# Performance work log

Measured on AMD Instinct MI355X. Metric: run time of the kernel, lower is better.

Reference implementation:

```python
import jax, jax.numpy as jnp
import numpy as np

NUM_HEADS = 16
HEAD_SIZE = 64
EMB = NUM_HEADS * HEAD_SIZE
B, S = 2, 2048


def setup_inputs() -> dict:
    key = jax.random.key(0)
    ks = jax.random.split(key, 8)
    return {
        "values": jax.random.normal(ks[0], (B, S, EMB), dtype=jnp.float32),
        "keys": jax.random.normal(ks[1], (B, S, EMB), dtype=jnp.float32),
        "queries": jax.random.normal(ks[2], (B, S, EMB), dtype=jnp.float32),
        "mask": jnp.ones((B, 1, 1, S), dtype=jnp.int32),
        "Wq": jax.random.normal(ks[3], (HEAD_SIZE, HEAD_SIZE), dtype=jnp.float32) / np.sqrt(HEAD_SIZE),
        "Wk": jax.random.normal(ks[4], (HEAD_SIZE, HEAD_SIZE), dtype=jnp.float32) / np.sqrt(HEAD_SIZE),
        "Wv": jax.random.normal(ks[5], (HEAD_SIZE, HEAD_SIZE), dtype=jnp.float32) / np.sqrt(HEAD_SIZE),
        "Wout": jax.random.normal(ks[6], (EMB, EMB), dtype=jnp.float32) / np.sqrt(EMB),
        "bout": jax.random.normal(ks[7], (EMB,), dtype=jnp.float32) * 0.01,
    }


def reference(values, keys, queries, mask, Wq, Wk, Wv, Wout, bout):
    n, q_len, E = queries.shape
    H, D = NUM_HEADS, HEAD_SIZE
    # split heads: [n, len, H, D]
    v = values.reshape(n, -1, H, D)
    k = keys.reshape(n, -1, H, D)
    q = queries.reshape(n, q_len, H, D)
    # per-head shared linears (torch Linear: x @ W.T), no bias
    v = jnp.einsum("nkhd,cd->nkhc", v, Wv)
    k = jnp.einsum("nkhd,cd->nkhc", k, Wk)
    q = jnp.einsum("nqhd,cd->nqhc", q, Wq)
    # scores: [n, H, q, k]
    energy = jnp.einsum("nqhd,nkhd->nhqk", q, k)
    energy = jnp.where(mask == 0, jnp.float32(-1e28), energy)
    # NOTE: source scales by sqrt(embedding_size), not head_size
    attn = jax.nn.softmax(energy / jnp.sqrt(jnp.float32(E)), axis=3)
    out = jnp.einsum("nhqk,nkhd->nqhd", attn, v).reshape(n, q_len, E)
    return out @ Wout.T + bout
```

## Files before the change

kernel.cpp:

```cpp
#include <hip/hip_runtime.h>
#include <hip/hip_bf16.h>


#define NHB 16
#define HS  64
#define EMB 1024
#define BB  2
#define SS  2048
#define NT  (SS / 64)

typedef __bf16 bf16_t;
typedef bf16_t bf16x8 __attribute__((ext_vector_type(8)));
typedef bf16_t bf16x4 __attribute__((ext_vector_type(4)));
typedef float  f32x4  __attribute__((ext_vector_type(4)));

__device__ __forceinline__ f32x4 mfma16(bf16x8 a, bf16x8 b, f32x4 c) {
    return __builtin_amdgcn_mfma_f32_16x16x32_bf16(a, b, c, 0, 0, 0);
}

__device__ __forceinline__ float fast_exp2(float x) {
#if __has_builtin(__builtin_amdgcn_exp2f)
    return __builtin_amdgcn_exp2f(x);
#else
    float r;
    asm("v_exp_f32 %0, %1" : "=v"(r) : "v"(x));
    return r;
#endif
}

__global__ __launch_bounds__(512) void proj_kernel(
    const float* __restrict__ queries, const float* __restrict__ keys,
    const float* __restrict__ values,
    const float* __restrict__ Wq, const float* __restrict__ Wk,
    const float* __restrict__ Wv,
    bf16_t* __restrict__ Qb, bf16_t* __restrict__ Kb, bf16_t* __restrict__ Vt)
{
    __shared__ bf16_t Ws[3][64][72];
    __shared__ bf16_t Xs[128][72];

    const int tid  = threadIdx.x;
    const int wave = tid >> 6, lane = tid & 63;
    const int q4 = lane >> 4, l16 = lane & 15;
    const int s0 = blockIdx.x * 128;
    const int h  = blockIdx.y, n = blockIdx.z;

    #pragma unroll
    for (int i = 0; i < 6; ++i) {
        int g = i * 512 + tid;
        int mW = g >> 10;
        int idx4 = g & 1023;
        const float* wp = (mW == 0) ? Wq : (mW == 1) ? Wk : Wv;
        float4 v = ((const float4*)wp)[idx4];
        int r = idx4 >> 4, c = (idx4 & 15) * 4;
        Ws[mW][r][c+0] = (bf16_t)v.x; Ws[mW][r][c+1] = (bf16_t)v.y;
        Ws[mW][r][c+2] = (bf16_t)v.z; Ws[mW][r][c+3] = (bf16_t)v.w;
    }

    const size_t headBase = (size_t)(n * NHB + h) * SS * HS;

    float4 gx[4];
    auto loadX = [&](const float* xp) {
        #pragma unroll
        for (int i = 0; i < 4; ++i) {
            int idx4 = i * 512 + tid;
            int r = idx4 >> 4, c = (idx4 & 15) * 4;
            gx[i] = *(const float4*)&xp[((size_t)(n * SS + s0 + r)) * EMB + h * HS + c];
        }
    };
    loadX(queries);

    for (int p = 0; p < 3; ++p) {
        __syncthreads();
        #pragma unroll
        for (int i = 0; i < 4; ++i) {
            int idx4 = i * 512 + tid;
            int r = idx4 >> 4, c = (idx4 & 15) * 4;
            Xs[r][c+0] = (bf16_t)gx[i].x; Xs[r][c+1] = (bf16_t)gx[i].y;
            Xs[r][c+2] = (bf16_t)gx[i].z; Xs[r][c+3] = (bf16_t)gx[i].w;
        }
        if (p == 0) loadX(keys);
        else if (p == 1) loadX(values);
        __syncthreads();

        bf16x8 xf[2], wf[4][2];
        #pragma unroll
        for (int kk = 0; kk < 2; ++kk)
            xf[kk] = *(const bf16x8*)&Xs[wave * 16 + l16][kk * 32 + q4 * 8];
        #pragma unroll
        for (int ct = 0; ct < 4; ++ct)
            #pragma unroll
            for (int kk = 0; kk < 2; ++kk)
                wf[ct][kk] = *(const bf16x8*)&Ws[p][ct * 16 + l16][kk * 32 + q4 * 8];

        if (p < 2) {
            bf16_t* dst = (p == 0) ? Qb : Kb;
            const float sc = (p == 0) ? (0.03125f * 1.44269504f) : 1.0f;
            bf16x8 lo, hi;
            #pragma unroll
            for (int ct = 0; ct < 4; ++ct) {
                f32x4 acc = {};
                acc = mfma16(wf[ct][0], xf[0], acc);
                acc = mfma16(wf[ct][1], xf[1], acc);
                #pragma unroll
                for (int i = 0; i < 4; ++i) {
                    bf16_t v = (bf16_t)(acc[i] * sc);
                    if (ct < 2) lo[ct * 4 + i] = v;
                    else        hi[(ct - 2) * 4 + i] = v;
                }
            }
            bf16_t* rp = dst + headBase
                + (size_t)(s0 + wave * 16 + l16) * HS + q4 * 16;
            *(bf16x8*)rp = lo;
            *(bf16x8*)(rp + 8) = hi;
        } else {
            #pragma unroll
            for (int ct = 0; ct < 4; ++ct) {
                f32x4 acc = {};
                acc = mfma16(xf[0], wf[ct][0], acc);
                acc = mfma16(xf[1], wf[ct][1], acc);
                bf16x4 pk;
                #pragma unroll
                for (int i = 0; i < 4; ++i) pk[i] = (bf16_t)acc[i];
                *(bf16x4*)&Vt[headBase + (size_t)(ct * 16 + l16) * SS
                              + s0 + (wave >> 1) * 32 + q4 * 8 + (wave & 1) * 4] = pk;
            }
        }
    }
}

__global__ __launch_bounds__(512) void attn_kernel(
    const bf16_t* __restrict__ Qb, const bf16_t* __restrict__ Kb,
    const bf16_t* __restrict__ Vt, const int* __restrict__ mask,
    bf16_t* __restrict__ Og)
{
    __shared__ __align__(16) unsigned char smem[37376];
    auto Ks = (bf16_t(*)[64][72])(smem);
    auto Vs = (bf16_t(*)[64][72])(smem + 18432);
    auto Ms = (float(*)[64])(smem + 36864);
    float* fbuf = (float*)smem;
    float* lbuf = (float*)(smem + 32768);

    const int tid = threadIdx.x;
    const int w = tid >> 6, lane = tid & 63;
    const int q4 = lane >> 4, l16 = lane & 15;
    const int wq = w & 3, wk = w >> 2;
    const int qt = blockIdx.x, h = blockIdx.y, n = blockIdx.z;
    const size_t headBase = (size_t)(n * NHB + h) * SS * HS;
    const int* mrow = mask + n * SS;

    const int sr = tid >> 3, sc = (tid & 7) * 8;
    const bf16_t* kb_src = Kb + headBase + (size_t)sr * HS + sc;
    const bf16_t* vt_src = Vt + headBase + (size_t)sr * SS + sc;

    bf16x8 bq[2][2];
    #pragma unroll
    for (int st = 0; st < 2; ++st) {
        const bf16_t* qptr = Qb + headBase
            + (size_t)(qt * 128 + wq * 32 + st * 16 + l16) * HS;
        bq[st][0] = *(const bf16x8*)&qptr[q4 * 8];
        bq[st][1] = *(const bf16x8*)&qptr[32 + q4 * 8];
    }

    bf16x8 ones;
    #pragma unroll
    for (int i = 0; i < 8; ++i) ones[i] = (bf16_t)1.0f;

    f32x4 oaccT[2][4] = {};
    f32x4 lacc[2] = {};

    *(bf16x8*)&Ks[0][sr][sc] = *(const bf16x8*)kb_src;
    *(bf16x8*)&Vs[0][sr][sc] = *(const bf16x8*)vt_src;
    if (tid < 64) Ms[0][tid] = mrow[tid] ? 0.0f : -3e38f;
    __syncthreads();

    for (int kt = 0; kt < NT; ++kt) {
        const int cur = kt & 1;
        const bool has_next = (kt + 1) < NT;
        bf16x8 gk, gv; float gm = 0.f;
        if (has_next) {
            const int k0n = (kt + 1) * 64;
            gk = *(const bf16x8*)(kb_src + (size_t)k0n * HS);
            gv = *(const bf16x8*)(vt_src + k0n);
            if (tid < 64) gm = mrow[k0n + tid] ? 0.0f : -3e38f;
        }

        f32x4 sacc[2][2];
        #pragma unroll
        for (int c2 = 0; c2 < 2; ++c2) {
            const int ct = wk * 2 + c2;
            float4 bias = *(const float4*)&Ms[cur][ct * 16 + q4 * 4];
            f32x4 b4 = {bias.x, bias.y, bias.z, bias.w};
            sacc[0][c2] = b4; sacc[1][c2] = b4;
            bf16x8 ak0 = *(const bf16x8*)&Ks[cur][ct * 16 + l16][q4 * 8];
            bf16x8 ak1 = *(const bf16x8*)&Ks[cur][ct * 16 + l16][32 + q4 * 8];
            #pragma unroll
            for (int st = 0; st < 2; ++st) {
                sacc[st][c2] = mfma16(ak0, bq[st][0], sacc[st][c2]);
                sacc[st][c2] = mfma16(ak1, bq[st][1], sacc[st][c2]);
            }
        }

        bf16x4 pv[2][2];
        #pragma unroll
        for (int c2 = 0; c2 < 2; ++c2)
            #pragma unroll
            for (int st = 0; st < 2; ++st) {
                bf16x4 pk;
                #pragma unroll
                for (int j = 0; j < 4; ++j)
                    pk[j] = (bf16_t)fast_exp2(sacc[st][c2][j]);
                pv[st][c2] = pk;
            }

        bf16x8 pa[2];
        #pragma unroll
        for (int st = 0; st < 2; ++st)
            pa[st] = __builtin_shufflevector(pv[st][0], pv[st][1],
                                             0, 1, 2, 3, 4, 5, 6, 7);
        #pragma unroll
        for (int dt = 0; dt < 4; ++dt) {
            bf16x8 av = *(const bf16x8*)&Vs[cur][dt * 16 + l16][wk * 32 + q4 * 8];
            oaccT[0][dt] = mfma16(av, pa[0], oaccT[0][dt]);
            oaccT[1][dt] = mfma16(av, pa[1], oaccT[1][dt]);
        }
        lacc[0] = mfma16(ones, pa[0], lacc[0]);
        lacc[1] = mfma16(ones, pa[1], lacc[1]);

        if (has_next) {
            const int nxt = 1 - cur;
            *(bf16x8*)&Ks[nxt][sr][sc] = gk;
            *(bf16x8*)&Vs[nxt][sr][sc] = gv;
            if (tid < 64) Ms[nxt][tid] = gm;
        }
        __syncthreads();
    }

    float ls[2] = {lacc[0][0], lacc[1][0]};

    if (w >= 4) {
        const int lanecol = wq * 64 + lane;
        #pragma unroll
        for (int st = 0; st < 2; ++st) {
            #pragma unroll
            for (int dt = 0; dt < 4; ++dt)
                #pragma unroll
                for (int j = 0; j < 4; ++j)
                    fbuf[(st * 16 + dt * 4 + j) * 256 + lanecol] = oaccT[st][dt][j];
            lbuf[st * 256 + lanecol] = ls[st];
        }
    }
    __syncthreads();
    if (w < 4) {
        const int lanecol = wq * 64 + lane;
        #pragma unroll
        for (int st = 0; st < 2; ++st) {
            #pragma unroll
            for (int dt = 0; dt < 4; ++dt)
                #pragma unroll
                for (int j = 0; j < 4; ++j)
                    oaccT[st][dt][j] += fbuf[(st * 16 + dt * 4 + j) * 256 + lanecol];
            ls[st] += lbuf[st * 256 + lanecol];
        }
        #pragma unroll
        for (int st = 0; st < 2; ++st) {
            const float inv = 1.f / ls[st];
            const int qrow = qt * 128 + wq * 32 + st * 16 + l16;
            bf16_t* obase = Og + ((size_t)(n * SS + qrow)) * EMB + h * HS;
            #pragma unroll
            for (int dt = 0; dt < 4; ++dt) {
                bf16x4 ov;
                #pragma unroll
                for (int j = 0; j < 4; ++j) ov[j] = (bf16_t)(oaccT[st][dt][j] * inv);
                *(bf16x4*)&obase[dt * 16 + q4 * 4] = ov;
            }
        }
    }
}

__global__ __launch_bounds__(512) void outproj_kernel(
    const bf16_t* __restrict__ Og, const float* __restrict__ Wout,
    const float* __restrict__ bout, float* __restrict__ out)
{
    __shared__ bf16_t As[2][128][72];
    __shared__ bf16_t Bs[2][64][72];
    const int tid = threadIdx.x;
    const int w = tid >> 6, lane = tid & 63;
    const int q4 = lane >> 4, l16 = lane & 15;
    const int wr = w >> 1, wc = w & 1;
    const int t0 = blockIdx.x * 128, c0 = blockIdx.y * 64;

    const int sr0 = tid >> 3, sc0 = (tid & 7) * 8;
    const int sr1 = sr0 + 64;
    const bf16_t* a0 = Og + (size_t)(t0 + sr0) * EMB + sc0;
    const bf16_t* a1 = Og + (size_t)(t0 + sr1) * EMB + sc0;
    const float*  b0 = Wout + (size_t)(c0 + sr0) * EMB + sc0;

    auto cvt8 = [](float4 x, float4 y) {
        bf16x8 r;
        r[0] = (bf16_t)x.x; r[1] = (bf16_t)x.y; r[2] = (bf16_t)x.z; r[3] = (bf16_t)x.w;
        r[4] = (bf16_t)y.x; r[5] = (bf16_t)y.y; r[6] = (bf16_t)y.z; r[7] = (bf16_t)y.w;
        return r;
    };

    f32x4 acc[2][2] = {};

    *(bf16x8*)&As[0][sr0][sc0] = *(const bf16x8*)a0;
    *(bf16x8*)&As[0][sr1][sc0] = *(const bf16x8*)a1;
    *(bf16x8*)&Bs[0][sr0][sc0] = cvt8(*(const float4*)b0, *(const float4*)(b0 + 4));
    __syncthreads();

    const int NE = EMB / 64;
    for (int et = 0; et < NE; ++et) {
        const int cur = et & 1;
        const bool has_next = (et + 1) < NE;
        bf16x8 ga0, ga1; float4 gb0, gb1;
        if (has_next) {
            const int e0 = (et + 1) * 64;
            ga0 = *(const bf16x8*)(a0 + e0); ga1 = *(const bf16x8*)(a1 + e0);
            gb0 = *(const float4*)(b0 + e0); gb1 = *(const float4*)(b0 + e0 + 4);
        }

        bf16x8 af[2][2], bfr[2][2];
        #pragma unroll
        for (int st = 0; st < 2; ++st)
            #pragma unroll
            for (int kk = 0; kk < 2; ++kk)
                af[st][kk] = *(const bf16x8*)&As[cur][wr * 32 + st * 16 + l16][kk * 32 + q4 * 8];
        #pragma unroll
        for (int ct = 0; ct < 2; ++ct)
            #pragma unroll
            for (int kk = 0; kk < 2; ++kk)
                bfr[ct][kk] = *(const bf16x8*)&Bs[cur][wc * 32 + ct * 16 + l16][kk * 32 + q4 * 8];
        #pragma unroll
        for (int st = 0; st < 2; ++st)
            #pragma unroll
            for (int ct = 0; ct < 2; ++ct) {
                acc[st][ct] = mfma16(af[st][0], bfr[ct][0], acc[st][ct]);
                acc[st][ct] = mfma16(af[st][1], bfr[ct][1], acc[st][ct]);
            }

        if (has_next) {
            const int nxt = 1 - cur;
            *(bf16x8*)&As[nxt][sr0][sc0] = ga0;
            *(bf16x8*)&As[nxt][sr1][sc0] = ga1;
            *(bf16x8*)&Bs[nxt][sr0][sc0] = cvt8(gb0, gb1);
        }
        __syncthreads();
    }

    #pragma unroll
    for (int ct = 0; ct < 2; ++ct) {
        const int c = c0 + wc * 32 + ct * 16 + l16;
        const float bias = bout[c];
        #pragma unroll
        for (int st = 0; st < 2; ++st)
            #pragma unroll
            for (int i = 0; i < 4; ++i)
                out[(size_t)(t0 + wr * 32 + st * 16 + q4 * 4 + i) * EMB + c]
                    = acc[st][ct][i] + bias;
    }
}

extern "C" void kernel_launch(void* const* d_in, const int* in_sizes, int n_in,
                              void* d_out, int out_size, void* d_ws, size_t ws_size,
                              hipStream_t stream)
{
    const float* values  = (const float*)d_in[0];
    const float* keys    = (const float*)d_in[1];
    const float* queries = (const float*)d_in[2];
    const int*   mask    = (const int*)d_in[3];
    const float* Wq      = (const float*)d_in[4];
    const float* Wk      = (const float*)d_in[5];
    const float* Wv      = (const float*)d_in[6];
    const float* Wout    = (const float*)d_in[7];
    const float* bout    = (const float*)d_in[8];
    float* out = (float*)d_out;

    const size_t M8 = 8ull * 1024 * 1024;
    bf16_t* Qb = (bf16_t*)d_ws;
    bf16_t* Kb = (bf16_t*)((char*)d_ws + 1 * M8);
    bf16_t* Vt = (bf16_t*)((char*)d_ws + 2 * M8);
    bf16_t* Og = (bf16_t*)((char*)d_ws + 3 * M8);

    proj_kernel<<<dim3(SS / 128, NHB, BB), 512, 0, stream>>>(
        queries, keys, values, Wq, Wk, Wv, Qb, Kb, Vt);
    attn_kernel<<<dim3(SS / 128, NHB, BB), 512, 0, stream>>>(
        Qb, Kb, Vt, mask, Og);
    outproj_kernel<<<dim3((BB * SS) / 128, EMB / 64), 512, 0, stream>>>(
        Og, Wout, bout, out);
}
```

Measured before the change: 169.1 us.

## Split attention into 64-query blocks with 4-way key split and swizzled grid

Halves the query tile per block from 128 to 64 and splits each 64-key tile four ways across waves, so the grid grows from 512 to 1024 blocks. Block IDs are remapped so groups of eight consecutive blocks share a query tile across different heads. The PV product now uses 16x16x16 MFMAs, s_setprio is raised around the MFMA sections, launch bounds request higher occupancy, and a two-stage LDS reduction combines the four partial accumulators. This aims to improve CU occupancy and load balance, at the cost of reloading each K/V tile for twice as many blocks and adding more reduction synchronisation.

Measured after the change: 599.4 us. 254% more time.

```diff
diff --git a/kernel.cpp b/kernel.cpp
--- a/kernel.cpp
+++ b/kernel.cpp
@@ -13,9 +13,24 @@
 typedef bf16_t bf16x8 __attribute__((ext_vector_type(8)));
 typedef bf16_t bf16x4 __attribute__((ext_vector_type(4)));
 typedef float  f32x4  __attribute__((ext_vector_type(4)));
+typedef short  s16x4  __attribute__((ext_vector_type(4)));
 
 __device__ __forceinline__ f32x4 mfma16(bf16x8 a, bf16x8 b, f32x4 c) {
     return __builtin_amdgcn_mfma_f32_16x16x32_bf16(a, b, c, 0, 0, 0);
+}
+
+__device__ __forceinline__ f32x4 mfma16k16(bf16x4 a, bf16x4 b, f32x4 c) {
+#if __has_builtin(__builtin_amdgcn_mfma_f32_16x16x16_bf16)
+    return __builtin_amdgcn_mfma_f32_16x16x16_bf16(a, b, c, 0, 0, 0);
+#elif __has_builtin(__builtin_amdgcn_mfma_f32_16x16x16bf16_1k)
+    return __builtin_amdgcn_mfma_f32_16x16x16bf16_1k(
+        __builtin_bit_cast(s16x4, a), __builtin_bit_cast(s16x4, b), c, 0, 0, 0);
+#else
+    f32x4 d;
+    asm("v_mfma_f32_16x16x16_bf16 %0, %1, %2, %3"
+        : "=v"(d) : "v"(a), "v"(b), "v"(c));
+    return d;
+#endif
 }
 
 __device__ __forceinline__ float fast_exp2(float x) {
@@ -128,7 +143,7 @@
     }
 }
 
-__global__ __launch_bounds__(512) void attn_kernel(
+__global__ __launch_bounds__(512, 8) void attn_kernel(
     const bf16_t* __restrict__ Qb, const bf16_t* __restrict__ Kb,
     const bf16_t* __restrict__ Vt, const int* __restrict__ mask,
     bf16_t* __restrict__ Og)
@@ -143,8 +158,14 @@
     const int tid = threadIdx.x;
     const int w = tid >> 6, lane = tid & 63;
     const int q4 = lane >> 4, l16 = lane & 15;
-    const int wq = w & 3, wk = w >> 2;
-    const int qt = blockIdx.x, h = blockIdx.y, n = blockIdx.z;
+    const int wq = w & 1, wk = w >> 1;
+
+    const int bid = blockIdx.x;
+    const int r = bid & 7, t = bid >> 3;
+    const int gi = t >> 5, qt = t & 31;
+    const int g = gi * 8 + r;
+    const int h = g & 15, n = g >> 4;
+
     const size_t headBase = (size_t)(n * NHB + h) * SS * HS;
     const int* mrow = mask + n * SS;
 
@@ -156,14 +177,14 @@
     #pragma unroll
     for (int st = 0; st < 2; ++st) {
         const bf16_t* qptr = Qb + headBase
-            + (size_t)(qt * 128 + wq * 32 + st * 16 + l16) * HS;
+            + (size_t)(qt * 64 + wq * 32 + st * 16 + l16) * HS;
         bq[st][0] = *(const bf16x8*)&qptr[q4 * 8];
         bq[st][1] = *(const bf16x8*)&qptr[32 + q4 * 8];
     }
 
-    bf16x8 ones;
+    bf16x4 ones4;
     #pragma unroll
-    for (int i = 0; i < 8; ++i) ones[i] = (bf16_t)1.0f;
+    for (int i = 0; i < 4; ++i) ones4[i] = (bf16_t)1.0f;
 
     f32x4 oaccT[2][4] = {};
     f32x4 lacc[2] = {};
@@ -172,6 +193,8 @@
     *(bf16x8*)&Vs[0][sr][sc] = *(const bf16x8*)vt_src;
     if (tid < 64) Ms[0][tid] = mrow[tid] ? 0.0f : -3e38f;
     __syncthreads();
+
+    const int vcol = (wk >> 1) * 32 + (wk & 1) * 4 + q4 * 8;
 
     for (int kt = 0; kt < NT; ++kt) {
         const int cur = kt & 1;
@@ -184,47 +207,36 @@
             if (tid < 64) gm = mrow[k0n + tid] ? 0.0f : -3e38f;
         }
 
-        f32x4 sacc[2][2];
-        #pragma unroll
-        for (int c2 = 0; c2 < 2; ++c2) {
-            const int ct = wk * 2 + c2;
-            float4 bias = *(const float4*)&Ms[cur][ct * 16 + q4 * 4];
-            f32x4 b4 = {bias.x, bias.y, bias.z, bias.w};
-            sacc[0][c2] = b4; sacc[1][c2] = b4;
-            bf16x8 ak0 = *(const bf16x8*)&Ks[cur][ct * 16 + l16][q4 * 8];
-            bf16x8 ak1 = *(const bf16x8*)&Ks[cur][ct * 16 + l16][32 + q4 * 8];
-            #pragma unroll
-            for (int st = 0; st < 2; ++st) {
-                sacc[st][c2] = mfma16(ak0, bq[st][0], sacc[st][c2]);
-                sacc[st][c2] = mfma16(ak1, bq[st][1], sacc[st][c2]);
-            }
-        }
-
-        bf16x4 pv[2][2];
-        #pragma unroll
-        for (int c2 = 0; c2 < 2; ++c2)
-            #pragma unroll
-            for (int st = 0; st < 2; ++st) {
-                bf16x4 pk;
-                #pragma unroll
-                for (int j = 0; j < 4; ++j)
-                    pk[j] = (bf16_t)fast_exp2(sacc[st][c2][j]);
-                pv[st][c2] = pk;
-            }
-
-        bf16x8 pa[2];
+        bf16x8 ak0 = *(const bf16x8*)&Ks[cur][wk * 16 + l16][q4 * 8];
+        bf16x8 ak1 = *(const bf16x8*)&Ks[cur][wk * 16 + l16][32 + q4 * 8];
+        float4 bias = *(const float4*)&Ms[cur][wk * 16 + q4 * 4];
+        f32x4 b4 = {bias.x, bias.y, bias.z, bias.w};
+        f32x4 sacc[2];
+        __builtin_amdgcn_s_setprio(1);
+        #pragma unroll
+        for (int st = 0; st < 2; ++st) {
+            f32x4 s = mfma16(ak0, bq[st][0], b4);
+            sacc[st] = mfma16(ak1, bq[st][1], s);
+        }
+        __builtin_amdgcn_s_setprio(0);
+
+        bf16x4 pv16[2];
         #pragma unroll
         for (int st = 0; st < 2; ++st)
-            pa[st] = __builtin_shufflevector(pv[st][0], pv[st][1],
-                                             0, 1, 2, 3, 4, 5, 6, 7);
+            #pragma unroll
+            for (int j = 0; j < 4; ++j)
+                pv16[st][j] = (bf16_t)fast_exp2(sacc[st][j]);
+
+        __builtin_amdgcn_s_setprio(1);
         #pragma unroll
         for (int dt = 0; dt < 4; ++dt) {
-            bf16x8 av = *(const bf16x8*)&Vs[cur][dt * 16 + l16][wk * 32 + q4 * 8];
-            oaccT[0][dt] = mfma16(av, pa[0], oaccT[0][dt]);
-            oaccT[1][dt] = mfma16(av, pa[1], oaccT[1][dt]);
-        }
-        lacc[0] = mfma16(ones, pa[0], lacc[0]);
-        lacc[1] = mfma16(ones, pa[1], lacc[1]);
+            bf16x4 av = *(const bf16x4*)&Vs[cur][dt * 16 + l16][vcol];
+            oaccT[0][dt] = mfma16k16(av, pv16[0], oaccT[0][dt]);
+            oaccT[1][dt] = mfma16k16(av, pv16[1], oaccT[1][dt]);
+        }
+        lacc[0] = mfma16k16(ones4, pv16[0], lacc[0]);
+        lacc[1] = mfma16k16(ones4, pv16[1], lacc[1]);
+        __builtin_amdgcn_s_setprio(0);
 
         if (has_next) {
             const int nxt = 1 - cur;
@@ -237,34 +249,58 @@
 
     float ls[2] = {lacc[0][0], lacc[1][0]};
 
-    if (w >= 4) {
-        const int lanecol = wq * 64 + lane;
+    if (wk >= 2) {
+        const int cg = wq * 2 + (wk - 2);
         #pragma unroll
         for (int st = 0; st < 2; ++st) {
             #pragma unroll
             for (int dt = 0; dt < 4; ++dt)
                 #pragma unroll
                 for (int j = 0; j < 4; ++j)
-                    fbuf[(st * 16 + dt * 4 + j) * 256 + lanecol] = oaccT[st][dt][j];
-            lbuf[st * 256 + lanecol] = ls[st];
+                    fbuf[(st * 16 + dt * 4 + j) * 256 + cg * 64 + lane] = oaccT[st][dt][j];
+            lbuf[st * 256 + cg * 64 + lane] = ls[st];
         }
     }
     __syncthreads();
-    if (w < 4) {
-        const int lanecol = wq * 64 + lane;
+    if (wk < 2) {
+        const int cg = wq * 2 + wk;
         #pragma unroll
         for (int st = 0; st < 2; ++st) {
             #pragma unroll
             for (int dt = 0; dt < 4; ++dt)
                 #pragma unroll
                 for (int j = 0; j < 4; ++j)
-                    oaccT[st][dt][j] += fbuf[(st * 16 + dt * 4 + j) * 256 + lanecol];
-            ls[st] += lbuf[st * 256 + lanecol];
+                    oaccT[st][dt][j] += fbuf[(st * 16 + dt * 4 + j) * 256 + cg * 64 + lane];
+            ls[st] += lbuf[st * 256 + cg * 64 + lane];
+        }
+    }
+    __syncthreads();
+    if (wk == 1) {
+        #pragma unroll
+        for (int st = 0; st < 2; ++st) {
+            #pragma unroll
+            for (int dt = 0; dt < 4; ++dt)
+                #pragma unroll
+                for (int j = 0; j < 4; ++j)
+                    fbuf[(st * 16 + dt * 4 + j) * 256 + wq * 64 + lane] = oaccT[st][dt][j];
+            lbuf[st * 256 + wq * 64 + lane] = ls[st];
+        }
+    }
+    __syncthreads();
+    if (wk == 0) {
+        #pragma unroll
+        for (int st = 0; st < 2; ++st) {
+            #pragma unroll
+            for (int dt = 0; dt < 4; ++dt)
+                #pragma unroll
+                for (int j = 0; j < 4; ++j)
+                    oaccT[st][dt][j] += fbuf[(st * 16 + dt * 4 + j) * 256 + wq * 64 + lane];
+            ls[st] += lbuf[st * 256 + wq * 64 + lane];
         }
         #pragma unroll
         for (int st = 0; st < 2; ++st) {
             const float inv = 1.f / ls[st];
-            const int qrow = qt * 128 + wq * 32 + st * 16 + l16;
+            const int qrow = qt * 64 + wq * 32 + st * 16 + l16;
             bf16_t* obase = Og + ((size_t)(n * SS + qrow)) * EMB + h * HS;
             #pragma unroll
             for (int dt = 0; dt < 4; ++dt) {
@@ -384,7 +420,7 @@
 
     proj_kernel<<<dim3(SS / 128, NHB, BB), 512, 0, stream>>>(
         queries, keys, values, Wq, Wk, Wv, Qb, Kb, Vt);
-    attn_kernel<<<dim3(SS / 128, NHB, BB), 512, 0, stream>>>(
+    attn_kernel<<<dim3(1024), 512, 0, stream>>>(
         Qb, Kb, Vt, mask, Og);
     outproj_kernel<<<dim3((BB * SS) / 128, EMB / 64), 512, 0, stream>>>(
         Og, Wout, bout, out);
```
